# Performance work log

Measured on AMD Instinct MI355X. Metric: run time of the kernel, lower is better.

The kernel has to match this reference:

```python
import jax, jax.numpy as jnp
import numpy as np

N, C, HW = 32, 256, 64          # batch, in_channels, input_size
K = 128                          # n_clusters
S = 8                            # blocks per side
BLOCK = (HW + S - 1) // S        # = 8, padding_size = 0


def setup_inputs() -> dict:
    key = jax.random.key(0)
    k1, k2 = jax.random.split(key)
    x = jax.random.normal(k1, (N, C, HW, HW), dtype=jnp.float32)
    cluster_centers = jax.random.normal(k2, (K, C), dtype=jnp.float32)
    return {"x": x, "cluster_centers": cluster_centers}


def reference(x, cluster_centers):
    # --- Codebook: argmin over squared distances, computed without the
    x2 = jnp.sum(x * x, axis=1)                       # (N, H, W)
    c2 = jnp.sum(cluster_centers * cluster_centers, axis=1)  # (K,)
    xc = jnp.einsum('nchw,kc->nkhw', x, cluster_centers)     # (N, K, H, W)
    dist = x2[:, None] - 2.0 * xc + c2[None, :, None, None]
    code = jnp.argmin(dist, axis=1)                   # (N, H, W) int

    # --- BlockWiseHistogramEncoder: unfold into S*S non-overlapping
    # BLOCKxBLOCK blocks (padding_size == 0 here), one_hot(code+1), mean ---
    shifted = code + 1                                # values in [1, K]
    n = shifted.shape[0]
    blocks = shifted.reshape(n, S, BLOCK, S, BLOCK)
    blocks = blocks.transpose(0, 1, 3, 2, 4).reshape(n, S * S, BLOCK * BLOCK)
    onehot = (blocks[..., None] == jnp.arange(K + 1)).astype(jnp.float32)
    return onehot.mean(axis=2)                        # (N, S*S, K+1)
```

## Files before the change

### kernel.cpp

```cpp
#include <hip/hip_runtime.h>

#define C_DIM 256
#define K_DIM 128
#define HW_DIM 64
#define PIX 4096
#define N_IMG 32

using short8 = __attribute__((ext_vector_type(8))) short;
using f32x4  = __attribute__((ext_vector_type(4))) float;

__device__ __forceinline__ void lds_barrier() {
    asm volatile("s_waitcnt lgkmcnt(0)\n\ts_barrier" ::: "memory");
}

__device__ __forceinline__ unsigned long long umin64(unsigned long long a, unsigned long long b) {
    return a < b ? a : b;
}
__device__ __forceinline__ unsigned mono(float d) {
    unsigned u = __float_as_uint(d);
    return u ^ ((u & 0x80000000u) ? 0xFFFFFFFFu : 0x80000000u);
}

__device__ __forceinline__ void split3t(float v, unsigned& hu, unsigned& mu, unsigned& lu) {
    unsigned u = __float_as_uint(v);
    unsigned hf = u & 0xffff0000u;
    float r1 = v - __uint_as_float(hf);
    unsigned r1u = __float_as_uint(r1);
    unsigned mf = r1u & 0xffff0000u;
    float r2 = r1 - __uint_as_float(mf);
    hu = u; mu = r1u; lu = __float_as_uint(r2);
}

__global__ __launch_bounds__(64) void prep_kernel(const float* __restrict__ cl,
                                                  unsigned short* __restrict__ Bt,
                                                  float* __restrict__ c2) {
    int k = blockIdx.x;
    int lane = threadIdx.x;
    const float4* row = (const float4*)(cl + k * C_DIM);
    float4 v = row[lane];
    float vv[4] = {v.x, v.y, v.z, v.w};
    unsigned short* bk = Bt + k * 768 + lane * 4;
#pragma unroll
    for (int i = 0; i < 4; ++i) {
        unsigned hu, mu, lu;
        split3t(vv[i], hu, mu, lu);
        bk[i]       = (unsigned short)(hu >> 16);
        bk[256 + i] = (unsigned short)(mu >> 16);
        bk[512 + i] = (unsigned short)(lu >> 16);
    }
    if (lane == 0) {
        float s = 0.f;
#pragma unroll
        for (int i = 0; i < C_DIM / 4; ++i) {
            float4 u = row[i];
            s = fmaf(u.x, u.x, s);
            s = fmaf(u.y, u.y, s);
            s = fmaf(u.z, u.z, s);
            s = fmaf(u.w, u.w, s);
        }
        c2[k] = s;
    }
}

__global__ __launch_bounds__(256, 4) void main_kernel(
    const float* __restrict__ x, const unsigned short* __restrict__ Bt,
    const float* __restrict__ c2v, float* __restrict__ out) {

    __shared__ __align__(16) unsigned short Ap[3 * 4096];
    __shared__ float x2p[2][128];
    unsigned long long* red = (unsigned long long*)Ap;

    const int t    = threadIdx.x;
    const int lane = t & 63;
    const int w    = t >> 6;
    const int q    = lane >> 4;
    const int l15  = lane & 15;

    const int px = t & 127;
    const int h  = t >> 7;

    const int b   = blockIdx.x;
    const int img = b >> 5;
    const int pb  = (b & 31) * 128;

    const float* xg = x + (size_t)img * (C_DIM * PIX) + pb + px;

    f32x4 acc[8][2];
#pragma unroll
    for (int m = 0; m < 8; ++m)
#pragma unroll
        for (int ns = 0; ns < 2; ++ns) acc[m][ns] = (f32x4){0.f, 0.f, 0.f, 0.f};

    float xr[16];
#pragma unroll
    for (int j = 0; j < 16; ++j) xr[j] = xg[(size_t)(h * 16 + j) * PIX];

    float x2part = 0.f;
    const unsigned short* btb = Bt + (w * 32 + l15) * 768 + q * 8;

    const int wbase = (px >> 4) * 512 + (px & 15) * 8 + h * 2 * 128;

#pragma unroll 1
    for (int ci = 0; ci < 8; ++ci) {
#pragma unroll
        for (int g = 0; g < 2; ++g) {
            unsigned p0[4], p1[4], p2[4];
#pragma unroll
            for (int jj = 0; jj < 4; ++jj) {
                float v0 = xr[g * 8 + jj * 2], v1 = xr[g * 8 + jj * 2 + 1];
                unsigned h0, m0, l0, h1, m1, l1;
                split3t(v0, h0, m0, l0);
                split3t(v1, m1, l1, h1);
                x2part = x2part;
                (void)p0; (void)p1; (void)p2;
                unsigned H0 = h0, M0 = m0, L0 = l0;
                unsigned H1, M1, L1;
                split3t(v1, H1, M1, L1);
                p0[jj] = __builtin_amdgcn_perm(H1, H0, 0x07060302u);
                p1[jj] = __builtin_amdgcn_perm(M1, M0, 0x07060302u);
                p2[jj] = __builtin_amdgcn_perm(L1, L0, 0x07060302u);
                x2part = fmaf(v0, v0, x2part);
                x2part = fmaf(v1, v1, x2part);
            }
            int base = wbase + g * 128;
            *(uint4*)&Ap[base]            = make_uint4(p0[0], p0[1], p0[2], p0[3]);
            *(uint4*)&Ap[4096 + base]     = make_uint4(p1[0], p1[1], p1[2], p1[3]);
            *(uint4*)&Ap[8192 + base]     = make_uint4(p2[0], p2[1], p2[2], p2[3]);
        }
        if (ci == 7) x2p[h][px] = x2part;

        short8 bv[3][2];
#pragma unroll
        for (int p = 0; p < 3; ++p) {
            bv[p][0] = *(const short8*)(btb + p * 256 + ci * 32);
            bv[p][1] = *(const short8*)(btb + 16 * 768 + p * 256 + ci * 32);
        }

        if (ci < 7) {
#pragma unroll
            for (int j = 0; j < 16; ++j)
                xr[j] = xg[(size_t)((ci + 1) * 32 + h * 16 + j) * PIX];
        }

        lds_barrier();

        __builtin_amdgcn_s_setprio(1);
#pragma unroll
        for (int pa = 0; pa < 3; ++pa) {
#pragma unroll
            for (int mg = 0; mg < 4; ++mg) {
                const int m0 = mg * 2, m1 = mg * 2 + 1;
                short8 af0 = *(const short8*)&Ap[pa * 4096 + m0 * 512 + lane * 8];
                short8 af1 = *(const short8*)&Ap[pa * 4096 + m1 * 512 + lane * 8];
#pragma unroll
                for (int pb2 = 0; pb2 < 3; ++pb2) {
                    if (pb2 < 3 - pa) {
                        acc[m0][0] = __builtin_amdgcn_mfma_f32_16x16x32_bf16(af0, bv[pb2][0], acc[m0][0], 0, 0, 0);
                        acc[m0][1] = __builtin_amdgcn_mfma_f32_16x16x32_bf16(af0, bv[pb2][1], acc[m0][1], 0, 0, 0);
                        acc[m1][0] = __builtin_amdgcn_mfma_f32_16x16x32_bf16(af1, bv[pb2][0], acc[m1][0], 0, 0, 0);
                        acc[m1][1] = __builtin_amdgcn_mfma_f32_16x16x32_bf16(af1, bv[pb2][1], acc[m1][1], 0, 0, 0);
                    }
                }
            }
        }
        __builtin_amdgcn_s_setprio(0);
        lds_barrier();
    }

    const float c2a0 = c2v[w * 32 + l15];
    const float c2a1 = c2v[w * 32 + 16 + l15];
    const unsigned n0 = (unsigned)(w * 32 + l15);
    const unsigned n1 = n0 + 16;

#pragma unroll
    for (int m = 0; m < 8; ++m) {
#pragma unroll
        for (int r = 0; r < 4; ++r) {
            int pxl = m * 16 + q * 4 + r;
            float x2v = x2p[0][pxl] + x2p[1][pxl];
            float d0 = (x2v - 2.0f * acc[m][0][r]) + c2a0;
            float d1 = (x2v - 2.0f * acc[m][1][r]) + c2a1;
            unsigned long long k0 = ((unsigned long long)mono(d0) << 32) | n0;
            unsigned long long k1 = ((unsigned long long)mono(d1) << 32) | n1;
            unsigned long long best = umin64(k0, k1);
            best = umin64(best, __shfl_xor(best, 1));
            best = umin64(best, __shfl_xor(best, 2));
            best = umin64(best, __shfl_xor(best, 4));
            best = umin64(best, __shfl_xor(best, 8));
            if (l15 == 0) red[w * 128 + pxl] = best;
        }
    }
    lds_barrier();

    if (t < 128) {
        unsigned long long m0 = umin64(umin64(red[t], red[128 + t]),
                                       umin64(red[256 + t], red[384 + t]));
        int c = (int)(m0 & 0xFFu);
        int p = pb + t;
        int sy = (p >> 6) >> 3;
        int sx = (p & 63) >> 3;
        atomicAdd(&out[(size_t)img * (64 * (K_DIM + 1)) +
                       (sy * 8 + sx) * (K_DIM + 1) + c + 1],
                  0.015625f);
    }
}

extern "C" void kernel_launch(void* const* d_in, const int* in_sizes, int n_in,
                              void* d_out, int out_size, void* d_ws, size_t ws_size,
                              hipStream_t stream) {
    const float* x  = (const float*)d_in[0];
    const float* cl = (const float*)d_in[1];
    float* out = (float*)d_out;

    unsigned short* Bt = (unsigned short*)d_ws;
    float* c2 = (float*)((char*)d_ws + 196608);

    hipMemsetAsync(d_out, 0, (size_t)out_size, stream);
    prep_kernel<<<K_DIM, 64, 0, stream>>>(cl, Bt, c2);
    main_kernel<<<(N_IMG * PIX) / 128, 256, 0, stream>>>(x, Bt, c2, out);
}
```

Measured before the change: 214.7 us.

## Build MFMA A fragments in registers per wave and drop LDS staging

The main kernel is restructured so each wave handles 16 pixels against all 128 clusters. The split-bf16 A fragments are built directly in registers from the loaded x values, which removes the LDS staging buffer and the two block barriers per channel chunk. The argmin now runs across eight accumulators in registers followed by a lane shuffle reduction, and atomics are issued straight from the waves. In exchange, every wave reloads the full split codebook from global/L2 for each channel chunk, which greatly increases B-operand traffic compared with the earlier per-block split.

```diff
diff --git a/kernel.cpp b/kernel.cpp
--- a/kernel.cpp
+++ b/kernel.cpp
@@ -8,10 +8,6 @@
 
 using short8 = __attribute__((ext_vector_type(8))) short;
 using f32x4  = __attribute__((ext_vector_type(4))) float;
-
-__device__ __forceinline__ void lds_barrier() {
-    asm volatile("s_waitcnt lgkmcnt(0)\n\ts_barrier" ::: "memory");
-}
 
 __device__ __forceinline__ unsigned long long umin64(unsigned long long a, unsigned long long b) {
     return a < b ? a : b;
@@ -51,7 +47,7 @@
     if (lane == 0) {
         float s = 0.f;
 #pragma unroll
-        for (int i = 0; i < C_DIM / 4; ++i) {
+    for (int i = 0; i < C_DIM / 4; ++i) {
             float4 u = row[i];
             s = fmaf(u.x, u.x, s);
             s = fmaf(u.y, u.y, s);
@@ -66,142 +62,124 @@
     const float* __restrict__ x, const unsigned short* __restrict__ Bt,
     const float* __restrict__ c2v, float* __restrict__ out) {
 
-    __shared__ __align__(16) unsigned short Ap[3 * 4096];
-    __shared__ float x2p[2][128];
-    unsigned long long* red = (unsigned long long*)Ap;
+    __shared__ float x2w[4][16];
 
     const int t    = threadIdx.x;
     const int lane = t & 63;
     const int w    = t >> 6;
-    const int q    = lane >> 4;
     const int l15  = lane & 15;
+    const int g    = lane >> 4;
 
-    const int px = t & 127;
-    const int h  = t >> 7;
+    const int gw  = blockIdx.x * 4 + w;
+    const int img = gw >> 8;
+    const int pxb = (gw & 255) * 16;
 
-    const int b   = blockIdx.x;
-    const int img = b >> 5;
-    const int pb  = (b & 31) * 128;
+    const float* xg = x + (size_t)img * (C_DIM * PIX) + pxb + l15;
+    const unsigned short* btv = Bt + l15 * 768 + g * 8;
 
-    const float* xg = x + (size_t)img * (C_DIM * PIX) + pb + px;
+    f32x4 acc[8];
+#pragma unroll
+    for (int kg = 0; kg < 8; ++kg) acc[kg] = (f32x4){0.f, 0.f, 0.f, 0.f};
 
-    f32x4 acc[8][2];
+    float xr[8];
 #pragma unroll
-    for (int m = 0; m < 8; ++m)
-#pragma unroll
-        for (int ns = 0; ns < 2; ++ns) acc[m][ns] = (f32x4){0.f, 0.f, 0.f, 0.f};
+    for (int j = 0; j < 8; ++j) xr[j] = xg[(size_t)(g * 8 + j) * PIX];
 
-    float xr[16];
-#pragma unroll
-    for (int j = 0; j < 16; ++j) xr[j] = xg[(size_t)(h * 16 + j) * PIX];
-
-    float x2part = 0.f;
-    const unsigned short* btb = Bt + (w * 32 + l15) * 768 + q * 8;
-
-    const int wbase = (px >> 4) * 512 + (px & 15) * 8 + h * 2 * 128;
+    float x2r = 0.f;
 
 #pragma unroll 1
     for (int ci = 0; ci < 8; ++ci) {
+        unsigned P0[4], P1[4], P2[4];
 #pragma unroll
-        for (int g = 0; g < 2; ++g) {
-            unsigned p0[4], p1[4], p2[4];
+        for (int jj = 0; jj < 4; ++jj) {
+            float v0 = xr[jj * 2], v1 = xr[jj * 2 + 1];
+            unsigned h0, m0, l0, h1, m1, l1;
+            split3t(v0, h0, m0, l0);
+            split3t(v1, h1, m1, l1);
+            P0[jj] = __builtin_amdgcn_perm(h1, h0, 0x07060302u);
+            P1[jj] = __builtin_amdgcn_perm(m1, m0, 0x07060302u);
+            P2[jj] = __builtin_amdgcn_perm(l1, l0, 0x07060302u);
+        }
+        union { uint4 u; short8 s; } A0, A1, A2;
+        A0.u = make_uint4(P0[0], P0[1], P0[2], P0[3]);
+        A1.u = make_uint4(P1[0], P1[1], P1[2], P1[3]);
+        A2.u = make_uint4(P2[0], P2[1], P2[2], P2[3]);
+        short8 af[3] = {A0.s, A1.s, A2.s};
+
+        float tA = x2r;
 #pragma unroll
-            for (int jj = 0; jj < 4; ++jj) {
-                float v0 = xr[g * 8 + jj * 2], v1 = xr[g * 8 + jj * 2 + 1];
-                unsigned h0, m0, l0, h1, m1, l1;
-                split3t(v0, h0, m0, l0);
-                split3t(v1, m1, l1, h1);
-                x2part = x2part;
-                (void)p0; (void)p1; (void)p2;
-                unsigned H0 = h0, M0 = m0, L0 = l0;
-                unsigned H1, M1, L1;
-                split3t(v1, H1, M1, L1);
-                p0[jj] = __builtin_amdgcn_perm(H1, H0, 0x07060302u);
-                p1[jj] = __builtin_amdgcn_perm(M1, M0, 0x07060302u);
-                p2[jj] = __builtin_amdgcn_perm(L1, L0, 0x07060302u);
-                x2part = fmaf(v0, v0, x2part);
-                x2part = fmaf(v1, v1, x2part);
-            }
-            int base = wbase + g * 128;
-            *(uint4*)&Ap[base]            = make_uint4(p0[0], p0[1], p0[2], p0[3]);
-            *(uint4*)&Ap[4096 + base]     = make_uint4(p1[0], p1[1], p1[2], p1[3]);
-            *(uint4*)&Ap[8192 + base]     = make_uint4(p2[0], p2[1], p2[2], p2[3]);
-        }
-        if (ci == 7) x2p[h][px] = x2part;
-
-        short8 bv[3][2];
+        for (int j = 0; j < 8; ++j) tA = fmaf(xr[j], xr[j], tA);
+        float ux = __shfl_xor(tA, 16);
+        float tB = ux;
 #pragma unroll
-        for (int p = 0; p < 3; ++p) {
-            bv[p][0] = *(const short8*)(btb + p * 256 + ci * 32);
-            bv[p][1] = *(const short8*)(btb + 16 * 768 + p * 256 + ci * 32);
-        }
+        for (int j = 0; j < 8; ++j) tB = fmaf(xr[j], xr[j], tB);
+        x2r = __shfl_xor(tB, 16);
 
         if (ci < 7) {
 #pragma unroll
-            for (int j = 0; j < 16; ++j)
-                xr[j] = xg[(size_t)((ci + 1) * 32 + h * 16 + j) * PIX];
+            for (int j = 0; j < 8; ++j)
+                xr[j] = xg[(size_t)((ci + 1) * 32 + g * 8 + j) * PIX];
         }
 
-        lds_barrier();
-
-        __builtin_amdgcn_s_setprio(1);
 #pragma unroll
-        for (int pa = 0; pa < 3; ++pa) {
+        for (int kq = 0; kq < 2; ++kq) {
+            short8 bq[4][3];
 #pragma unroll
-            for (int mg = 0; mg < 4; ++mg) {
-                const int m0 = mg * 2, m1 = mg * 2 + 1;
-                short8 af0 = *(const short8*)&Ap[pa * 4096 + m0 * 512 + lane * 8];
-                short8 af1 = *(const short8*)&Ap[pa * 4096 + m1 * 512 + lane * 8];
+            for (int kk = 0; kk < 4; ++kk)
+#pragma unroll
+                for (int p = 0; p < 3; ++p)
+                    bq[kk][p] = *(const short8*)(btv + (kq * 4 + kk) * 12288 +
+                                                 p * 256 + ci * 32);
+            __builtin_amdgcn_s_setprio(1);
+#pragma unroll
+            for (int pa = 0; pa < 3; ++pa)
 #pragma unroll
                 for (int pb2 = 0; pb2 < 3; ++pb2) {
                     if (pb2 < 3 - pa) {
-                        acc[m0][0] = __builtin_amdgcn_mfma_f32_16x16x32_bf16(af0, bv[pb2][0], acc[m0][0], 0, 0, 0);
-                        acc[m0][1] = __builtin_amdgcn_mfma_f32_16x16x32_bf16(af0, bv[pb2][1], acc[m0][1], 0, 0, 0);
-                        acc[m1][0] = __builtin_amdgcn_mfma_f32_16x16x32_bf16(af1, bv[pb2][0], acc[m1][0], 0, 0, 0);
-                        acc[m1][1] = __builtin_amdgcn_mfma_f32_16x16x32_bf16(af1, bv[pb2][1], acc[m1][1], 0, 0, 0);
+#pragma unroll
+                        for (int kk = 0; kk < 4; ++kk)
+                            acc[kq * 4 + kk] = __builtin_amdgcn_mfma_f32_16x16x32_bf16(
+                                af[pa], bq[kk][pb2], acc[kq * 4 + kk], 0, 0, 0);
                     }
                 }
-            }
+            __builtin_amdgcn_s_setprio(0);
         }
-        __builtin_amdgcn_s_setprio(0);
-        lds_barrier();
     }
 
-    const float c2a0 = c2v[w * 32 + l15];
-    const float c2a1 = c2v[w * 32 + 16 + l15];
-    const unsigned n0 = (unsigned)(w * 32 + l15);
-    const unsigned n1 = n0 + 16;
+    {
+        float x2o = __shfl_xor(x2r, 32);
+        if (g == 0) x2w[w][l15] = x2r + x2o;
+    }
+
+    float c2r[8];
+#pragma unroll
+    for (int kg = 0; kg < 8; ++kg) c2r[kg] = c2v[kg * 16 + l15];
+
+    const size_t ob = (size_t)img * (64 * (K_DIM + 1));
 
 #pragma unroll
-    for (int m = 0; m < 8; ++m) {
+    for (int r = 0; r < 4; ++r) {
+        float x2v = x2w[w][g * 4 + r];
+        unsigned long long best = 0xFFFFFFFFFFFFFFFFull;
 #pragma unroll
-        for (int r = 0; r < 4; ++r) {
-            int pxl = m * 16 + q * 4 + r;
-            float x2v = x2p[0][pxl] + x2p[1][pxl];
-            float d0 = (x2v - 2.0f * acc[m][0][r]) + c2a0;
-            float d1 = (x2v - 2.0f * acc[m][1][r]) + c2a1;
-            unsigned long long k0 = ((unsigned long long)mono(d0) << 32) | n0;
-            unsigned long long k1 = ((unsigned long long)mono(d1) << 32) | n1;
-            unsigned long long best = umin64(k0, k1);
-            best = umin64(best, __shfl_xor(best, 1));
-            best = umin64(best, __shfl_xor(best, 2));
-            best = umin64(best, __shfl_xor(best, 4));
-            best = umin64(best, __shfl_xor(best, 8));
-            if (l15 == 0) red[w * 128 + pxl] = best;
+        for (int kg = 0; kg < 8; ++kg) {
+            float d = (x2v - 2.0f * acc[kg][r]) + c2r[kg];
+            unsigned long long key =
+                ((unsigned long long)mono(d) << 32) | (unsigned)(kg * 16 + l15);
+            best = umin64(best, key);
         }
-    }
-    lds_barrier();
-
-    if (t < 128) {
-        unsigned long long m0 = umin64(umin64(red[t], red[128 + t]),
-                                       umin64(red[256 + t], red[384 + t]));
-        int c = (int)(m0 & 0xFFu);
-        int p = pb + t;
-        int sy = (p >> 6) >> 3;
-        int sx = (p & 63) >> 3;
-        atomicAdd(&out[(size_t)img * (64 * (K_DIM + 1)) +
-                       (sy * 8 + sx) * (K_DIM + 1) + c + 1],
-                  0.015625f);
+        best = umin64(best, __shfl_xor(best, 1));
+        best = umin64(best, __shfl_xor(best, 2));
+        best = umin64(best, __shfl_xor(best, 4));
+        best = umin64(best, __shfl_xor(best, 8));
+        if (l15 == 0) {
+            int c  = (int)(best & 0xFFu);
+            int p  = pxb + g * 4 + r;
+            int sy = (p >> 6) >> 3;
+            int sx = (p & 63) >> 3;
+            atomicAdd(&out[ob + (sy * 8 + sx) * (K_DIM + 1) + c + 1],
+                      0.015625f);
+        }
     }
 }
 
@@ -217,5 +195,5 @@
 
     hipMemsetAsync(d_out, 0, (size_t)out_size, stream);
     prep_kernel<<<K_DIM, 64, 0, stream>>>(cl, Bt, c2);
-    main_kernel<<<(N_IMG * PIX) / 128, 256, 0, stream>>>(x, Bt, c2, out);
+    main_kernel<<<(N_IMG * PIX) / 64, 256, 0, stream>>>(x, Bt, c2, out);
 }
```

Measured after the change: 342.5 us. +59.5%, slower.

## Halve pixels per block and double-buffer LDS A-tiles to overlap conversion with MFMA

Applied to the files above, without the earlier changes.

Each block now handles 64 pixels (one image row) instead of 128, so the grid doubles to 2048 blocks and per-wave accumulators halve. The A-operand LDS buffer is double-buffered, so the bf16 split conversion of the next channel chunk runs while MFMAs on the current chunk execute. This removes one barrier per iteration, and global loads are prefetched two chunks ahead. The x^2 reduction now goes through cross-lane shuffles, and the redundant triple split from the old code is gone. In exchange, each block reloads the B fragments, so B traffic doubles.

```diff
diff --git a/kernel.cpp b/kernel.cpp
--- a/kernel.cpp
+++ b/kernel.cpp
@@ -66,69 +66,69 @@
     const float* __restrict__ x, const unsigned short* __restrict__ Bt,
     const float* __restrict__ c2v, float* __restrict__ out) {
 
-    __shared__ __align__(16) unsigned short Ap[3 * 4096];
-    __shared__ float x2p[2][128];
-    unsigned long long* red = (unsigned long long*)Ap;
+    __shared__ __align__(16) unsigned short Ap[2][6144];
+    __shared__ float x2sh[64];
+    unsigned long long* red = (unsigned long long*)&Ap[0][0];
 
     const int t    = threadIdx.x;
     const int lane = t & 63;
     const int w    = t >> 6;
-    const int q    = lane >> 4;
     const int l15  = lane & 15;
-
-    const int px = t & 127;
-    const int h  = t >> 7;
-
-    const int b   = blockIdx.x;
-    const int img = b >> 5;
-    const int pb  = (b & 31) * 128;
-
-    const float* xg = x + (size_t)img * (C_DIM * PIX) + pb + px;
-
-    f32x4 acc[8][2];
-#pragma unroll
-    for (int m = 0; m < 8; ++m)
+    const int g    = lane >> 4;
+
+    const int gb  = blockIdx.x;
+    const int img = gb >> 6;
+    const int pb  = (gb & 63) * 64;
+
+    const float* xg = x + (size_t)img * (C_DIM * PIX) + pb + w * 16 + l15;
+    const unsigned short* btb = Bt + (w * 32 + l15) * 768 + g * 8;
+
+    f32x4 acc[4][2];
+#pragma unroll
+    for (int m = 0; m < 4; ++m)
 #pragma unroll
         for (int ns = 0; ns < 2; ++ns) acc[m][ns] = (f32x4){0.f, 0.f, 0.f, 0.f};
 
-    float xr[16];
-#pragma unroll
-    for (int j = 0; j < 16; ++j) xr[j] = xg[(size_t)(h * 16 + j) * PIX];
-
-    float x2part = 0.f;
-    const unsigned short* btb = Bt + (w * 32 + l15) * 768 + q * 8;
-
-    const int wbase = (px >> 4) * 512 + (px & 15) * 8 + h * 2 * 128;
+    float xr[8];
+#pragma unroll
+    for (int j = 0; j < 8; ++j) xr[j] = xg[(size_t)(g * 8 + j) * PIX];
+
+    float x2r = 0.f;
+    const int wbase = w * 512 + g * 128 + l15 * 8;
+
+#define CONVERT_CHUNK(dst)                                                    \
+    {                                                                         \
+        unsigned P0[4], P1[4], P2[4];                                         \
+        _Pragma("unroll")                                                     \
+        for (int jj = 0; jj < 4; ++jj) {                                      \
+            float v0 = xr[jj * 2], v1 = xr[jj * 2 + 1];                       \
+            unsigned h0, m0, l0, h1, m1, l1;                                  \
+            split3t(v0, h0, m0, l0);                                          \
+            split3t(v1, h1, m1, l1);                                          \
+            P0[jj] = __builtin_amdgcn_perm(h1, h0, 0x07060302u);              \
+            P1[jj] = __builtin_amdgcn_perm(m1, m0, 0x07060302u);              \
+            P2[jj] = __builtin_amdgcn_perm(l1, l0, 0x07060302u);              \
+        }                                                                     \
+        *(uint4*)&(dst)[wbase]        = make_uint4(P0[0], P0[1], P0[2], P0[3]);\
+        *(uint4*)&(dst)[2048 + wbase] = make_uint4(P1[0], P1[1], P1[2], P1[3]);\
+        *(uint4*)&(dst)[4096 + wbase] = make_uint4(P2[0], P2[1], P2[2], P2[3]);\
+        float tA = x2r;                                                       \
+        _Pragma("unroll")                                                     \
+        for (int j = 0; j < 8; ++j) tA = fmaf(xr[j], xr[j], tA);              \
+        float ux = __shfl_xor(tA, 16);                                        \
+        float tB = ux;                                                        \
+        _Pragma("unroll")                                                     \
+        for (int j = 0; j < 8; ++j) tB = fmaf(xr[j], xr[j], tB);              \
+        x2r = __shfl_xor(tB, 16);                                             \
+    }
+
+    CONVERT_CHUNK(Ap[0])
+#pragma unroll
+    for (int j = 0; j < 8; ++j) xr[j] = xg[(size_t)(32 + g * 8 + j) * PIX];
+    lds_barrier();
 
 #pragma unroll 1
     for (int ci = 0; ci < 8; ++ci) {
-#pragma unroll
-        for (int g = 0; g < 2; ++g) {
-            unsigned p0[4], p1[4], p2[4];
-#pragma unroll
-            for (int jj = 0; jj < 4; ++jj) {
-                float v0 = xr[g * 8 + jj * 2], v1 = xr[g * 8 + jj * 2 + 1];
-                unsigned h0, m0, l0, h1, m1, l1;
-                split3t(v0, h0, m0, l0);
-                split3t(v1, m1, l1, h1);
-                x2part = x2part;
-                (void)p0; (void)p1; (void)p2;
-                unsigned H0 = h0, M0 = m0, L0 = l0;
-                unsigned H1, M1, L1;
-                split3t(v1, H1, M1, L1);
-                p0[jj] = __builtin_amdgcn_perm(H1, H0, 0x07060302u);
-                p1[jj] = __builtin_amdgcn_perm(M1, M0, 0x07060302u);
-                p2[jj] = __builtin_amdgcn_perm(L1, L0, 0x07060302u);
-                x2part = fmaf(v0, v0, x2part);
-                x2part = fmaf(v1, v1, x2part);
-            }
-            int base = wbase + g * 128;
-            *(uint4*)&Ap[base]            = make_uint4(p0[0], p0[1], p0[2], p0[3]);
-            *(uint4*)&Ap[4096 + base]     = make_uint4(p1[0], p1[1], p1[2], p1[3]);
-            *(uint4*)&Ap[8192 + base]     = make_uint4(p2[0], p2[1], p2[2], p2[3]);
-        }
-        if (ci == 7) x2p[h][px] = x2part;
-
         short8 bv[3][2];
 #pragma unroll
         for (int p = 0; p < 3; ++p) {
@@ -136,36 +136,40 @@
             bv[p][1] = *(const short8*)(btb + 16 * 768 + p * 256 + ci * 32);
         }
 
-        if (ci < 7) {
-#pragma unroll
-            for (int j = 0; j < 16; ++j)
-                xr[j] = xg[(size_t)((ci + 1) * 32 + h * 16 + j) * PIX];
-        }
-
-        lds_barrier();
-
+        if (ci < 7) CONVERT_CHUNK(Ap[(ci + 1) & 1])
+
+        if (ci < 6) {
+#pragma unroll
+            for (int j = 0; j < 8; ++j)
+                xr[j] = xg[(size_t)((ci + 2) * 32 + g * 8 + j) * PIX];
+        }
+
+        const unsigned short* ap = &Ap[ci & 1][0];
         __builtin_amdgcn_s_setprio(1);
 #pragma unroll
         for (int pa = 0; pa < 3; ++pa) {
 #pragma unroll
-            for (int mg = 0; mg < 4; ++mg) {
-                const int m0 = mg * 2, m1 = mg * 2 + 1;
-                short8 af0 = *(const short8*)&Ap[pa * 4096 + m0 * 512 + lane * 8];
-                short8 af1 = *(const short8*)&Ap[pa * 4096 + m1 * 512 + lane * 8];
+            for (int m = 0; m < 4; ++m) {
+                short8 af = *(const short8*)&ap[pa * 2048 + m * 512 + lane * 8];
 #pragma unroll
                 for (int pb2 = 0; pb2 < 3; ++pb2) {
                     if (pb2 < 3 - pa) {
-                        acc[m0][0] = __builtin_amdgcn_mfma_f32_16x16x32_bf16(af0, bv[pb2][0], acc[m0][0], 0, 0, 0);
-                        acc[m0][1] = __builtin_amdgcn_mfma_f32_16x16x32_bf16(af0, bv[pb2][1], acc[m0][1], 0, 0, 0);
-                        acc[m1][0] = __builtin_amdgcn_mfma_f32_16x16x32_bf16(af1, bv[pb2][0], acc[m1][0], 0, 0, 0);
-                        acc[m1][1] = __builtin_amdgcn_mfma_f32_16x16x32_bf16(af1, bv[pb2][1], acc[m1][1], 0, 0, 0);
+                        acc[m][0] = __builtin_amdgcn_mfma_f32_16x16x32_bf16(af, bv[pb2][0], acc[m][0], 0, 0, 0);
+                        acc[m][1] = __builtin_amdgcn_mfma_f32_16x16x32_bf16(af, bv[pb2][1], acc[m][1], 0, 0, 0);
                     }
                 }
             }
         }
         __builtin_amdgcn_s_setprio(0);
-        lds_barrier();
-    }
+
+        if (ci < 7) lds_barrier();
+    }
+
+    {
+        float x2o = __shfl_xor(x2r, 32);
+        if (g == 0) x2sh[w * 16 + l15] = x2r + x2o;
+    }
+    lds_barrier();
 
     const float c2a0 = c2v[w * 32 + l15];
     const float c2a1 = c2v[w * 32 + 16 + l15];
@@ -173,11 +177,11 @@
     const unsigned n1 = n0 + 16;
 
 #pragma unroll
-    for (int m = 0; m < 8; ++m) {
+    for (int m = 0; m < 4; ++m) {
 #pragma unroll
         for (int r = 0; r < 4; ++r) {
-            int pxl = m * 16 + q * 4 + r;
-            float x2v = x2p[0][pxl] + x2p[1][pxl];
+            int pxl = m * 16 + g * 4 + r;
+            float x2v = x2sh[pxl];
             float d0 = (x2v - 2.0f * acc[m][0][r]) + c2a0;
             float d1 = (x2v - 2.0f * acc[m][1][r]) + c2a1;
             unsigned long long k0 = ((unsigned long long)mono(d0) << 32) | n0;
@@ -187,22 +191,22 @@
             best = umin64(best, __shfl_xor(best, 2));
             best = umin64(best, __shfl_xor(best, 4));
             best = umin64(best, __shfl_xor(best, 8));
-            if (l15 == 0) red[w * 128 + pxl] = best;
+            if (l15 == 0) red[w * 64 + pxl] = best;
         }
     }
     lds_barrier();
 
-    if (t < 128) {
-        unsigned long long m0 = umin64(umin64(red[t], red[128 + t]),
-                                       umin64(red[256 + t], red[384 + t]));
-        int c = (int)(m0 & 0xFFu);
-        int p = pb + t;
-        int sy = (p >> 6) >> 3;
-        int sx = (p & 63) >> 3;
+    if (t < 64) {
+        unsigned long long m0 = umin64(umin64(red[t], red[64 + t]),
+                                       umin64(red[128 + t], red[192 + t]));
+        int c  = (int)(m0 & 0xFFu);
+        int sy = (gb & 63) >> 3;
+        int sx = t >> 3;
         atomicAdd(&out[(size_t)img * (64 * (K_DIM + 1)) +
                        (sy * 8 + sx) * (K_DIM + 1) + c + 1],
                   0.015625f);
     }
+#undef CONVERT_CHUNK
 }
 
 extern "C" void kernel_launch(void* const* d_in, const int* in_sizes, int n_in,
@@ -217,5 +221,5 @@
 
     hipMemsetAsync(d_out, 0, (size_t)out_size, stream);
     prep_kernel<<<K_DIM, 64, 0, stream>>>(cl, Bt, c2);
-    main_kernel<<<(N_IMG * PIX) / 128, 256, 0, stream>>>(x, Bt, c2, out);
-}
+    main_kernel<<<(N_IMG * PIX) / 64, 256, 0, stream>>>(x, Bt, c2, out);
+}
```

Result: slower. 228.6 us (+6.5%).
